# Kernel tuning notes

Measured on AMD Instinct MI355X. Metric: run time of the kernel, lower is better.

## Reference

```python
import jax, jax.numpy as jnp
import numpy as np

D_MODEL = 1024
NUM_HEADS = 16
HEAD_DIM = D_MODEL // NUM_HEADS


def setup_inputs() -> dict:
    key = jax.random.key(0)
    kx, kq, kk, kv, ko = jax.random.split(key, 5)
    init_std = float(np.sqrt(2.0 / (D_MODEL + D_MODEL)))
    def trunc(k):
        # trunc normal in [-3std, 3std], matching nn.init.trunc_normal_
        return jax.random.truncated_normal(k, -3.0, 3.0, (D_MODEL, D_MODEL), jnp.float32) * init_std
    return {
        "x": jax.random.normal(kx, (2, 2048, D_MODEL), jnp.float32),
        "Wq": trunc(kq),
        "Wk": trunc(kk),
        "Wv": trunc(kv),
        "Wo": trunc(ko),
    }


def reference(x, Wq, Wk, Wv, Wo):
    b, s, _ = x.shape
    # projections: Linear computes x @ W.T with W [out, in]
    q = (x @ Wq.T).reshape(b, s, NUM_HEADS, HEAD_DIM).transpose(0, 2, 1, 3)
    k = (x @ Wk.T).reshape(b, s, NUM_HEADS, HEAD_DIM).transpose(0, 2, 1, 3)
    v = (x @ Wv.T).reshape(b, s, NUM_HEADS, HEAD_DIM).transpose(0, 2, 1, 3)
    scale = 1.0 / jnp.sqrt(jnp.float32(HEAD_DIM))
    logits = jnp.einsum("bhqd,bhkd->bhqk", q, k)  # [b,h,s,s]
    causal = jnp.tril(jnp.ones((s, s), dtype=bool))
    logits = jnp.where(causal, logits, -jnp.inf)
    attn = jax.nn.softmax(logits * scale, axis=-1)
    out = jnp.einsum("bhqk,bhkd->bhqd", attn, v)
    out = out.transpose(0, 2, 1, 3).reshape(b, s, D_MODEL)
    return out @ Wo.T
```

## Files before the change

kernel.cpp:

```cpp
#include <hip/hip_runtime.h>
#include <hip/hip_bf16.h>


#define DEVI __device__ __forceinline__

typedef __bf16 bf16x8 __attribute__((ext_vector_type(8)));
typedef short  short8 __attribute__((ext_vector_type(8)));
typedef float  f32x4  __attribute__((ext_vector_type(4)));
typedef float  f32x16 __attribute__((ext_vector_type(16)));
typedef unsigned int u32x4 __attribute__((ext_vector_type(4)));

DEVI short f2bfs(float f) {
    __hip_bfloat16 h = __float2bfloat16(f);
    return __builtin_bit_cast(short, h);
}
DEVI unsigned pack2rb(float a, float b) {
    const unsigned ua = __builtin_bit_cast(unsigned, a) + 0x8000u;
    const unsigned ub = __builtin_bit_cast(unsigned, b) + 0x8000u;
    return __builtin_amdgcn_perm(ub, ua, 0x07060302u);
}
DEVI bf16x8 ld8(const short* p) {
    return __builtin_bit_cast(bf16x8, *(const short8*)p);
}
DEVI void gload16(const void* g, void* lds) {
    __builtin_amdgcn_global_load_lds(
        (const __attribute__((address_space(1))) void*)g,
        (__attribute__((address_space(3))) void*)lds, 16, 0, 0);
}
DEVI void plswap(unsigned& a, unsigned& b) {
    asm volatile("v_permlane32_swap_b32 %0, %1" : "+v"(a), "+v"(b));
}
DEVI const short* lds_swc(const short* base, int row, int col) {
    return (const short*)((const char*)base + (((row << 7) + (col << 1)) ^ ((row & 7) << 4)));
}

#if defined(__has_builtin)
#if __has_builtin(__builtin_amdgcn_exp2f)
#define HAVE_EXP2 1
#endif
#endif
DEVI float ex2(float x) {
#ifdef HAVE_EXP2
    return __builtin_amdgcn_exp2f(x);
#else
    return __expf(x * 0.69314718055994531f);
#endif
}
#define CEXP 0.18033688011112042f
#define MCF  (64.0f * CEXP)

__global__ __launch_bounds__(256) void convert_kernel(
    const float* __restrict__ x, const float* __restrict__ Wq,
    const float* __restrict__ Wk, const float* __restrict__ Wv,
    const float* __restrict__ Wo, short* __restrict__ xb, short* __restrict__ wb) {
    const int bid = blockIdx.x;
    const float* src;
    short* dst;
    int i8;
    if (bid < 2048) {
        src = x; dst = xb;
        i8 = (bid * 256 + threadIdx.x) * 8;
    } else {
        const int w = bid - 2048;
        const int z = w >> 9;
        src = (z == 0) ? Wq : (z == 1) ? Wk : (z == 2) ? Wv : Wo;
        dst = wb + (size_t)z * 1048576;
        i8 = (((w & 511) * 256) + threadIdx.x) * 8;
    }
    float4 a = ((const float4*)(src + i8))[0];
    float4 b = ((const float4*)(src + i8))[1];
    short8 t;
    t[0] = f2bfs(a.x); t[1] = f2bfs(a.y); t[2] = f2bfs(a.z); t[3] = f2bfs(a.w);
    t[4] = f2bfs(b.x); t[5] = f2bfs(b.y); t[6] = f2bfs(b.z); t[7] = f2bfs(b.w);
    *(short8*)(dst + i8) = t;
}

template <int BM, int BN, int MF, int NF, int WN>
DEVI void gemm_kloop64(const short* __restrict__ A, const short* __restrict__ B,
                       short* As, short* Bs, int wid, int lane, f32x4 acc[MF][NF]) {
    const int l15 = lane & 15, l4 = lane >> 4;
    const int wm = wid / WN, wn = wid % WN;
    const int rowc = lane >> 3;
    const int gcol = ((lane & 7) ^ rowc) * 8;
    constexpr int NCHA = BM / 8, NCHB = BN / 8;
#pragma unroll 1
    for (int k0 = 0; k0 < 1024; k0 += 64) {
        __syncthreads();
#pragma unroll
        for (int c = wid; c < NCHA; c += 4)
            gload16(A + (size_t)(c * 8 + rowc) * 1024 + k0 + gcol, As + c * 512);
#pragma unroll
        for (int c = wid; c < NCHB; c += 4)
            gload16(B + (size_t)(c * 8 + rowc) * 1024 + k0 + gcol, Bs + c * 512);
        __syncthreads();
#pragma unroll
        for (int kk = 0; kk < 2; ++kk) {
            bf16x8 af[MF], bf[NF];
#pragma unroll
            for (int m = 0; m < MF; ++m) {
                const int row = wm * (MF * 16) + m * 16 + l15;
                af[m] = ld8(As + row * 64 + (((kk * 4 + l4) ^ (row & 7)) * 8));
            }
#pragma unroll
            for (int n = 0; n < NF; ++n) {
                const int row = wn * (NF * 16) + n * 16 + l15;
                bf[n] = ld8(Bs + row * 64 + (((kk * 4 + l4) ^ (row & 7)) * 8));
            }
#pragma unroll
            for (int m = 0; m < MF; ++m)
#pragma unroll
                for (int n = 0; n < NF; ++n)
                    acc[m][n] = __builtin_amdgcn_mfma_f32_16x16x32_bf16(af[m], bf[n], acc[m][n], 0, 0, 0);
        }
    }
}

__global__ __launch_bounds__(256) void gemm_qkv_kernel(
    const short* __restrict__ xb, const short* __restrict__ wb,
    short* __restrict__ Qo, short* __restrict__ Ko, short* __restrict__ VtG) {
    __shared__ short As[8192], Bs[8192];
    const int tid = threadIdx.x, lane = tid & 63, wid = tid >> 6;
    const int l15 = lane & 15, l4 = lane >> 4;
    const int wm = wid >> 1, wn = wid & 1;
    const int y = blockIdx.y, wsel = y >> 3;
    const int row0 = blockIdx.x * 128, col0 = (y & 7) * 128;

    f32x4 acc[4][4] = {};
    gemm_kloop64<128, 128, 4, 4, 2>(
        xb + (size_t)row0 * 1024,
        wb + (size_t)wsel * 1048576 + (size_t)col0 * 1024,
        As, Bs, wid, lane, acc);

    if (wsel == 2) {
#pragma unroll
        for (int m = 0; m < 4; ++m)
#pragma unroll
            for (int n = 0; n < 4; ++n)
#pragma unroll
                for (int j = 0; j < 4; ++j) {
                    int row = row0 + wm * 64 + m * 16 + l4 * 4 + j;
                    int col = col0 + wn * 64 + n * 16 + l15;
                    VtG[(size_t)col * 4096 + row] = f2bfs(acc[m][n][j]);
                }
    } else {
        short* C = (wsel == 0) ? Qo : Ko;
#pragma unroll
        for (int m = 0; m < 4; ++m)
#pragma unroll
            for (int n = 0; n < 4; ++n)
#pragma unroll
                for (int j = 0; j < 4; ++j) {
                    int row = row0 + wm * 64 + m * 16 + l4 * 4 + j;
                    int col = col0 + wn * 64 + n * 16 + l15;
                    C[(size_t)row * 1024 + col] = f2bfs(acc[m][n][j]);
                }
    }
}

__global__ __launch_bounds__(256) void gemm_wo_kernel(
    const short* __restrict__ Ao, const short* __restrict__ Wob,
    float* __restrict__ Cout) {
    __shared__ short As[4096], Bs[8192];
    const int tid = threadIdx.x, lane = tid & 63, wid = tid >> 6;
    const int l15 = lane & 15, l4 = lane >> 4;
    const int wn = wid;
    const int row0 = blockIdx.x * 64, col0 = blockIdx.y * 128;

    f32x4 acc[4][2] = {};
    gemm_kloop64<64, 128, 4, 2, 4>(
        Ao + (size_t)row0 * 1024, Wob + (size_t)col0 * 1024,
        As, Bs, wid, lane, acc);

#pragma unroll
    for (int m = 0; m < 4; ++m)
#pragma unroll
        for (int n = 0; n < 2; ++n)
#pragma unroll
            for (int j = 0; j < 4; ++j) {
                int row = row0 + m * 16 + l4 * 4 + j;
                int col = col0 + wn * 32 + n * 16 + l15;
                Cout[(size_t)row * 1024 + col] = acc[m][n][j];
            }
}

DEVI void read_frags(const short* Ks, const short* Vts, int l31, int hi,
                     bf16x8 kf[8], bf16x8 vb[8]) {
#pragma unroll
    for (int ds = 0; ds < 4; ++ds) {
        kf[ds]     = ld8(lds_swc(Ks, l31,      ds * 16 + hi * 8));
        kf[4 + ds] = ld8(lds_swc(Ks, 32 + l31, ds * 16 + hi * 8));
    }
#pragma unroll
    for (int c = 0; c < 2; ++c) {
        vb[c * 4 + 0] = ld8(lds_swc(Vts, l31,      c * 32 + hi * 8));
        vb[c * 4 + 1] = ld8(lds_swc(Vts, 32 + l31, c * 32 + hi * 8));
        vb[c * 4 + 2] = ld8(lds_swc(Vts, l31,      c * 32 + 16 + hi * 8));
        vb[c * 4 + 3] = ld8(lds_swc(Vts, 32 + l31, c * 32 + 16 + hi * 8));
    }
}

template <bool DIAG>
DEVI void attn_tile_r(int kv0, const bf16x8 kf[8], const bf16x8 vb[8],
                      const bf16x8 qf[4], f32x16& o0, f32x16& o1,
                      float& l, int qrow, int hi) {
    f32x16 s0 = 0.0f, s1 = 0.0f;
    __builtin_amdgcn_s_setprio(1);
#pragma unroll
    for (int ds = 0; ds < 4; ++ds)
        s0 = __builtin_amdgcn_mfma_f32_32x32x16_bf16(kf[ds], qf[ds], s0, 0, 0, 0);
#pragma unroll
    for (int ds = 0; ds < 4; ++ds)
        s1 = __builtin_amdgcn_mfma_f32_32x32x16_bf16(kf[4 + ds], qf[ds], s1, 0, 0, 0);
    __builtin_amdgcn_s_setprio(0);

    if (DIAG) {
#pragma unroll
        for (int r = 0; r < 16; ++r) {
            const int kvr = kv0 + (r & 3) + 8 * (r >> 2) + 4 * hi;
            if (kvr > qrow)      s0[r] = -3.0e38f;
            if (kvr + 32 > qrow) s1[r] = -3.0e38f;
        }
    }

    float r0 = 0.f, r1 = 0.f, r2 = 0.f, r3 = 0.f;
    unsigned w0[8], w1[8];
#pragma unroll
    for (int i = 0; i < 8; ++i) {
        const float p0 = ex2(__builtin_fmaf(s0[2 * i],     CEXP, -MCF));
        const float p1 = ex2(__builtin_fmaf(s0[2 * i + 1], CEXP, -MCF));
        const float p2 = ex2(__builtin_fmaf(s1[2 * i],     CEXP, -MCF));
        const float p3 = ex2(__builtin_fmaf(s1[2 * i + 1], CEXP, -MCF));
        r0 += p0; r1 += p1; r2 += p2; r3 += p3;
        w0[i] = pack2rb(p0, p1);
        w1[i] = pack2rb(p2, p3);
    }
    l += (r0 + r1) + (r2 + r3);

    __builtin_amdgcn_s_setprio(1);
#pragma unroll
    for (int c = 0; c < 2; ++c) {
        const unsigned* w = (c == 0) ? w0 : w1;
        unsigned a0 = w[0], a2 = w[2]; plswap(a0, a2);
        unsigned a1 = w[1], a3 = w[3]; plswap(a1, a3);
        unsigned a4 = w[4], a6 = w[6]; plswap(a4, a6);
        unsigned a5 = w[5], a7 = w[7]; plswap(a5, a7);
        u32x4 lo, hw;
        lo[0] = a0; lo[1] = a1; lo[2] = a2; lo[3] = a3;
        hw[0] = a4; hw[1] = a5; hw[2] = a6; hw[3] = a7;
        const bf16x8 paL = __builtin_bit_cast(bf16x8, lo);
        const bf16x8 paH = __builtin_bit_cast(bf16x8, hw);

        o0 = __builtin_amdgcn_mfma_f32_32x32x16_bf16(paL, vb[c * 4 + 0], o0, 0, 0, 0);
        o1 = __builtin_amdgcn_mfma_f32_32x32x16_bf16(paL, vb[c * 4 + 1], o1, 0, 0, 0);
        o0 = __builtin_amdgcn_mfma_f32_32x32x16_bf16(paH, vb[c * 4 + 2], o0, 0, 0, 0);
        o1 = __builtin_amdgcn_mfma_f32_32x32x16_bf16(paH, vb[c * 4 + 3], o1, 0, 0, 0);
    }
    __builtin_amdgcn_s_setprio(0);
}

__global__ __launch_bounds__(128) void attn_kernel(
    const short* __restrict__ Q, const short* __restrict__ K,
    const short* __restrict__ VtG, short* __restrict__ O) {
    __shared__ short KsA[4096], VtsA[4096], KsB[4096], VtsB[4096];

    const int tid = threadIdx.x, lane = tid & 63, wid = tid >> 6;
    const int l31 = lane & 31, hi = lane >> 5;
    const int bid = blockIdx.x;
    const int qt = 31 - (bid >> 5);
    const int bh = bid & 31;
    const int b = bh >> 4, h = bh & 15;
    const size_t base = (size_t)b * 2048 * 1024 + (size_t)h * 64;
    const short* Qp = Q + base;
    const short* Kp = K + base;
    const short* Vp = VtG + (size_t)(h * 64) * 4096 + (size_t)b * 2048;
    short* Op = O + base;

    const int q0w = qt * 64 + wid * 32;
    const int qrow = q0w + l31;

    const int srw = lane >> 3;
    const int swc = ((lane & 7) ^ srw) * 8;
    const short* kSrc = Kp + (size_t)srw * 1024 + swc;
    const short* vSrc = Vp + (size_t)srw * 4096 + swc;
    const int cc0 = wid * 4;

#define ISSUE_TILE(Ksb, Vtsb, kv0_)                                           \
    {                                                                         \
        const int kv0i = (kv0_);                                              \
        _Pragma("unroll")                                                     \
        for (int c = 0; c < 4; ++c) {                                         \
            const int cc = cc0 + c;                                           \
            gload16(kSrc + (size_t)(kv0i + cc * 8) * 1024, (Ksb) + cc * 512); \
            gload16(vSrc + (size_t)(cc * 8) * 4096 + kv0i, (Vtsb) + cc * 512);\
        }                                                                     \
    }

    const int nt = qt + 1;

    ISSUE_TILE(KsA, VtsA, 0);

    bf16x8 qf[4];
#pragma unroll
    for (int ds = 0; ds < 4; ++ds)
        qf[ds] = ld8(Qp + (size_t)qrow * 1024 + ds * 16 + hi * 8);

    asm volatile("s_waitcnt vmcnt(0)" ::: "memory");
    __builtin_amdgcn_s_barrier();
    __builtin_amdgcn_sched_barrier(0);

    if (nt > 1) ISSUE_TILE(KsB, VtsB, 64);
    bf16x8 kf[8], vb[8];
    read_frags(KsA, VtsA, l31, hi, kf, vb);
    __builtin_amdgcn_sched_barrier(0);

    f32x16 o0 = 0.0f, o1 = 0.0f;
    float l = 0.0f;

#pragma unroll 1
    for (int t = 0; t < nt - 1; ++t) {
        attn_tile_r<false>(t * 64, kf, vb, qf, o0, o1, l, qrow, hi);
        asm volatile("s_waitcnt lgkmcnt(0) vmcnt(0)" ::: "memory");
        __builtin_amdgcn_s_barrier();
        __builtin_amdgcn_sched_barrier(0);
        if (t + 2 < nt) {
            short* Kso  = (t & 1) ? KsB  : KsA;
            short* Vtso = (t & 1) ? VtsB : VtsA;
            ISSUE_TILE(Kso, Vtso, (t + 2) * 64);
        }
        const short* Ksn  = (t & 1) ? KsA  : KsB;
        const short* Vtsn = (t & 1) ? VtsA : VtsB;
        read_frags(Ksn, Vtsn, l31, hi, kf, vb);
        __builtin_amdgcn_sched_barrier(0);
    }

    attn_tile_r<true>((nt - 1) * 64, kf, vb, qf, o0, o1, l, qrow, hi);
#undef ISSUE_TILE

    const float lt = l + __shfl_xor(l, 32, 64);
    const float il = 1.0f / lt;
#pragma unroll
    for (int r = 0; r < 16; ++r) {
        const int cr = (r & 3) + 8 * (r >> 2) + 4 * hi;
        const float s = __shfl(il, cr, 64);
        const size_t row = (size_t)(q0w + cr) * 1024;
        Op[row + l31]      = f2bfs(o0[r] * s);
        Op[row + 32 + l31] = f2bfs(o1[r] * s);
    }
}

extern "C" void kernel_launch(void* const* d_in, const int* in_sizes, int n_in,
                              void* d_out, int out_size, void* d_ws, size_t ws_size,
                              hipStream_t stream) {
    const float* x  = (const float*)d_in[0];
    const float* Wq = (const float*)d_in[1];
    const float* Wk = (const float*)d_in[2];
    const float* Wv = (const float*)d_in[3];
    const float* Wo = (const float*)d_in[4];

    short* wb  = (short*)d_ws;
    short* Qw  = wb + (size_t)4 * 1048576;
    short* Kw  = Qw + (size_t)4194304;
    short* Vtw = Kw + (size_t)4194304;
    short* xb  = (short*)d_out;

    convert_kernel<<<4096, 256, 0, stream>>>(x, Wq, Wk, Wv, Wo, xb, wb);
    gemm_qkv_kernel<<<dim3(32, 24), 256, 0, stream>>>(xb, wb, Qw, Kw, Vtw);
    attn_kernel<<<1024, 128, 0, stream>>>(Qw, Kw, Vtw, Qw);
    gemm_wo_kernel<<<dim3(64, 8), 256, 0, stream>>>(Qw, wb + (size_t)3 * 1048576, (float*)d_out);
}
```

Measured before the change: 116.1 us.

## Double-buffer GEMM k-loop and retile QKV projection with XCD-aware block mapping

The GEMM inner loop now double-buffers LDS tiles, issuing the next k-slice's global-to-LDS loads before computing on the current one, with a single barrier per iteration. The QKV kernel switches to 128x192 tiles over the fused 3072-wide weight matrix, launched as a 1D grid of 512 blocks. Blocks are remapped so that neighbouring column tiles land on the same XCD, and the epilogue routes each column to Q, K or transposed V. This costs more LDS (80KB dynamic) and more accumulator registers, which may reduce occupancy.

```diff
diff --git a/kernel.cpp b/kernel.cpp
--- a/kernel.cpp
+++ b/kernel.cpp
@@ -76,35 +76,51 @@
 }
 
 template <int BM, int BN, int MF, int NF, int WN>
-DEVI void gemm_kloop64(const short* __restrict__ A, const short* __restrict__ B,
-                       short* As, short* Bs, int wid, int lane, f32x4 acc[MF][NF]) {
+DEVI void gemm_kloop64_db(const short* __restrict__ A, const short* __restrict__ B,
+                          short* As0, short* Bs0, short* As1, short* Bs1,
+                          int wid, int lane, f32x4 acc[MF][NF]) {
     const int l15 = lane & 15, l4 = lane >> 4;
     const int wm = wid / WN, wn = wid % WN;
     const int rowc = lane >> 3;
     const int gcol = ((lane & 7) ^ rowc) * 8;
     constexpr int NCHA = BM / 8, NCHB = BN / 8;
+
+#define GISSUE(As_, Bs_, k0_)                                                  \
+    {                                                                          \
+        _Pragma("unroll")                                                      \
+        for (int c = wid; c < NCHA; c += 4)                                    \
+            gload16(A + (size_t)(c * 8 + rowc) * 1024 + (k0_) + gcol, (As_) + c * 512); \
+        _Pragma("unroll")                                                      \
+        for (int c = wid; c < NCHB; c += 4)                                    \
+            gload16(B + (size_t)(c * 8 + rowc) * 1024 + (k0_) + gcol, (Bs_) + c * 512); \
+    }
+
+    GISSUE(As0, Bs0, 0);
+    asm volatile("s_waitcnt vmcnt(0)" ::: "memory");
+    __builtin_amdgcn_s_barrier();
+    __builtin_amdgcn_sched_barrier(0);
+
 #pragma unroll 1
-    for (int k0 = 0; k0 < 1024; k0 += 64) {
-        __syncthreads();
-#pragma unroll
-        for (int c = wid; c < NCHA; c += 4)
-            gload16(A + (size_t)(c * 8 + rowc) * 1024 + k0 + gcol, As + c * 512);
-#pragma unroll
-        for (int c = wid; c < NCHB; c += 4)
-            gload16(B + (size_t)(c * 8 + rowc) * 1024 + k0 + gcol, Bs + c * 512);
-        __syncthreads();
+    for (int k = 0; k < 16; ++k) {
+        if (k + 1 < 16) {
+            short* Asn = (k & 1) ? As0 : As1;
+            short* Bsn = (k & 1) ? Bs0 : Bs1;
+            GISSUE(Asn, Bsn, (k + 1) * 64);
+        }
+        const short* Asc = (k & 1) ? As1 : As0;
+        const short* Bsc = (k & 1) ? Bs1 : Bs0;
 #pragma unroll
         for (int kk = 0; kk < 2; ++kk) {
             bf16x8 af[MF], bf[NF];
 #pragma unroll
             for (int m = 0; m < MF; ++m) {
                 const int row = wm * (MF * 16) + m * 16 + l15;
-                af[m] = ld8(As + row * 64 + (((kk * 4 + l4) ^ (row & 7)) * 8));
+                af[m] = ld8(Asc + row * 64 + (((kk * 4 + l4) ^ (row & 7)) * 8));
             }
 #pragma unroll
             for (int n = 0; n < NF; ++n) {
                 const int row = wn * (NF * 16) + n * 16 + l15;
-                bf[n] = ld8(Bs + row * 64 + (((kk * 4 + l4) ^ (row & 7)) * 8));
+                bf[n] = ld8(Bsc + row * 64 + (((kk * 4 + l4) ^ (row & 7)) * 8));
             }
 #pragma unroll
             for (int m = 0; m < MF; ++m)
@@ -112,64 +128,64 @@
                 for (int n = 0; n < NF; ++n)
                     acc[m][n] = __builtin_amdgcn_mfma_f32_16x16x32_bf16(af[m], bf[n], acc[m][n], 0, 0, 0);
         }
-    }
+        asm volatile("s_waitcnt lgkmcnt(0) vmcnt(0)" ::: "memory");
+        __builtin_amdgcn_s_barrier();
+        __builtin_amdgcn_sched_barrier(0);
+    }
+#undef GISSUE
 }
 
 __global__ __launch_bounds__(256) void gemm_qkv_kernel(
     const short* __restrict__ xb, const short* __restrict__ wb,
     short* __restrict__ Qo, short* __restrict__ Ko, short* __restrict__ VtG) {
-    __shared__ short As[8192], Bs[8192];
+    extern __shared__ short smem[];
+    short* As0 = smem;
+    short* As1 = smem + 8192;
+    short* Bs0 = smem + 16384;
+    short* Bs1 = smem + 28672;
+
     const int tid = threadIdx.x, lane = tid & 63, wid = tid >> 6;
     const int l15 = lane & 15, l4 = lane >> 4;
     const int wm = wid >> 1, wn = wid & 1;
-    const int y = blockIdx.y, wsel = y >> 3;
-    const int row0 = blockIdx.x * 128, col0 = (y & 7) * 128;
-
-    f32x4 acc[4][4] = {};
-    gemm_kloop64<128, 128, 4, 4, 2>(
-        xb + (size_t)row0 * 1024,
-        wb + (size_t)wsel * 1048576 + (size_t)col0 * 1024,
-        As, Bs, wid, lane, acc);
-
-    if (wsel == 2) {
-#pragma unroll
-        for (int m = 0; m < 4; ++m)
-#pragma unroll
-            for (int n = 0; n < 4; ++n)
-#pragma unroll
-                for (int j = 0; j < 4; ++j) {
-                    int row = row0 + wm * 64 + m * 16 + l4 * 4 + j;
-                    int col = col0 + wn * 64 + n * 16 + l15;
-                    VtG[(size_t)col * 4096 + row] = f2bfs(acc[m][n][j]);
-                }
-    } else {
-        short* C = (wsel == 0) ? Qo : Ko;
-#pragma unroll
-        for (int m = 0; m < 4; ++m)
-#pragma unroll
-            for (int n = 0; n < 4; ++n)
-#pragma unroll
-                for (int j = 0; j < 4; ++j) {
-                    int row = row0 + wm * 64 + m * 16 + l4 * 4 + j;
-                    int col = col0 + wn * 64 + n * 16 + l15;
-                    C[(size_t)row * 1024 + col] = f2bfs(acc[m][n][j]);
-                }
-    }
+    const int bid = blockIdx.x;
+    const int xcd = bid & 7, idx = bid >> 3;
+    const int ytile = xcd * 2 + (idx & 1);
+    const int xtile = idx >> 1;
+    const int row0 = xtile * 128, col0 = ytile * 192;
+
+    f32x4 acc[4][6] = {};
+    gemm_kloop64_db<128, 192, 4, 6, 2>(
+        xb + (size_t)row0 * 1024, wb + (size_t)col0 * 1024,
+        As0, Bs0, As1, Bs1, wid, lane, acc);
+
+#pragma unroll
+    for (int m = 0; m < 4; ++m)
+#pragma unroll
+        for (int n = 0; n < 6; ++n)
+#pragma unroll
+            for (int j = 0; j < 4; ++j) {
+                const int row = row0 + wm * 64 + m * 16 + l4 * 4 + j;
+                const int col = col0 + wn * 96 + n * 16 + l15;
+                const short v = f2bfs(acc[m][n][j]);
+                if (col < 1024)       Qo[(size_t)row * 1024 + col] = v;
+                else if (col < 2048)  Ko[(size_t)row * 1024 + (col - 1024)] = v;
+                else                  VtG[(size_t)(col - 2048) * 4096 + row] = v;
+            }
 }
 
 __global__ __launch_bounds__(256) void gemm_wo_kernel(
     const short* __restrict__ Ao, const short* __restrict__ Wob,
     float* __restrict__ Cout) {
-    __shared__ short As[4096], Bs[8192];
+    __shared__ short As0[4096], As1[4096], Bs0[8192], Bs1[8192];
     const int tid = threadIdx.x, lane = tid & 63, wid = tid >> 6;
     const int l15 = lane & 15, l4 = lane >> 4;
     const int wn = wid;
     const int row0 = blockIdx.x * 64, col0 = blockIdx.y * 128;
 
     f32x4 acc[4][2] = {};
-    gemm_kloop64<64, 128, 4, 2, 4>(
+    gemm_kloop64_db<64, 128, 4, 2, 4>(
         Ao + (size_t)row0 * 1024, Wob + (size_t)col0 * 1024,
-        As, Bs, wid, lane, acc);
+        As0, Bs0, As1, Bs1, wid, lane, acc);
 
 #pragma unroll
     for (int m = 0; m < 4; ++m)
@@ -177,8 +193,8 @@
         for (int n = 0; n < 2; ++n)
 #pragma unroll
             for (int j = 0; j < 4; ++j) {
-                int row = row0 + m * 16 + l4 * 4 + j;
-                int col = col0 + wn * 32 + n * 16 + l15;
+                const int row = row0 + m * 16 + l4 * 4 + j;
+                const int col = col0 + wn * 32 + n * 16 + l15;
                 Cout[(size_t)row * 1024 + col] = acc[m][n][j];
             }
 }
@@ -364,7 +380,7 @@
     short* xb  = (short*)d_out;
 
     convert_kernel<<<4096, 256, 0, stream>>>(x, Wq, Wk, Wv, Wo, xb, wb);
-    gemm_qkv_kernel<<<dim3(32, 24), 256, 0, stream>>>(xb, wb, Qw, Kw, Vtw);
+    gemm_qkv_kernel<<<512, 256, 81920, stream>>>(xb, wb, Qw, Kw, Vtw);
     attn_kernel<<<1024, 128, 0, stream>>>(Qw, Kw, Vtw, Qw);
     gemm_wo_kernel<<<dim3(64, 8), 256, 0, stream>>>(Qw, wb + (size_t)3 * 1048576, (float*)d_out);
 }
```

Measured after the change: 127.2 us. 1.1x slower.

## Process two KV tiles per barrier with four-stage LDS ring

Applied to the files above, without the earlier changes.

The attention kernel now keeps four K/V tile buffers in LDS and handles two 64-key tiles per loop iteration, loading fragments for both before computing. This halves the number of waitcnt+barrier synchronisations per KV tile and prefetches two tiles ahead. In exchange LDS use doubles to 64KB per block and register pressure rises from holding two sets of K/V fragments, which may reduce occupancy or cause spills.

```diff
diff --git a/kernel.cpp b/kernel.cpp
--- a/kernel.cpp
+++ b/kernel.cpp
@@ -177,8 +177,8 @@
         for (int n = 0; n < 2; ++n)
 #pragma unroll
             for (int j = 0; j < 4; ++j) {
-                int row = row0 + m * 16 + l4 * 4 + j;
-                int col = col0 + wn * 32 + n * 16 + l15;
+                const int row = row0 + m * 16 + l4 * 4 + j;
+                const int col = col0 + wn * 32 + n * 16 + l15;
                 Cout[(size_t)row * 1024 + col] = acc[m][n][j];
             }
 }
@@ -261,7 +261,7 @@
 __global__ __launch_bounds__(128) void attn_kernel(
     const short* __restrict__ Q, const short* __restrict__ K,
     const short* __restrict__ VtG, short* __restrict__ O) {
-    __shared__ short KsA[4096], VtsA[4096], KsB[4096], VtsB[4096];
+    __shared__ short Kb[4][4096], Vb[4][4096];
 
     const int tid = threadIdx.x, lane = tid & 63, wid = tid >> 6;
     const int l31 = lane & 31, hi = lane >> 5;
@@ -284,20 +284,22 @@
     const short* vSrc = Vp + (size_t)srw * 4096 + swc;
     const int cc0 = wid * 4;
 
-#define ISSUE_TILE(Ksb, Vtsb, kv0_)                                           \
-    {                                                                         \
-        const int kv0i = (kv0_);                                              \
-        _Pragma("unroll")                                                     \
-        for (int c = 0; c < 4; ++c) {                                         \
-            const int cc = cc0 + c;                                           \
-            gload16(kSrc + (size_t)(kv0i + cc * 8) * 1024, (Ksb) + cc * 512); \
-            gload16(vSrc + (size_t)(cc * 8) * 4096 + kv0i, (Vtsb) + cc * 512);\
-        }                                                                     \
-    }
-
     const int nt = qt + 1;
 
-    ISSUE_TILE(KsA, VtsA, 0);
+#define ISS(i)                                                                 \
+    if ((i) < nt) {                                                            \
+        short* Ksb = Kb[(i) & 3];                                              \
+        short* Vsb = Vb[(i) & 3];                                              \
+        const int kv0i = (i) * 64;                                             \
+        _Pragma("unroll")                                                      \
+        for (int c = 0; c < 4; ++c) {                                          \
+            const int cc = cc0 + c;                                            \
+            gload16(kSrc + (size_t)(kv0i + cc * 8) * 1024, Ksb + cc * 512);    \
+            gload16(vSrc + (size_t)(cc * 8) * 4096 + kv0i, Vsb + cc * 512);    \
+        }                                                                      \
+    }
+
+    ISS(0); ISS(1);
 
     bf16x8 qf[4];
 #pragma unroll
@@ -308,33 +310,37 @@
     __builtin_amdgcn_s_barrier();
     __builtin_amdgcn_sched_barrier(0);
 
-    if (nt > 1) ISSUE_TILE(KsB, VtsB, 64);
-    bf16x8 kf[8], vb[8];
-    read_frags(KsA, VtsA, l31, hi, kf, vb);
+    bf16x8 kf0[8], vb0[8], kf1[8], vb1[8];
+    read_frags(Kb[0], Vb[0], l31, hi, kf0, vb0);
+    if (nt > 1) read_frags(Kb[1], Vb[1], l31, hi, kf1, vb1);
     __builtin_amdgcn_sched_barrier(0);
+    ISS(2); ISS(3);
 
     f32x16 o0 = 0.0f, o1 = 0.0f;
     float l = 0.0f;
 
+    int t = 0;
 #pragma unroll 1
-    for (int t = 0; t < nt - 1; ++t) {
-        attn_tile_r<false>(t * 64, kf, vb, qf, o0, o1, l, qrow, hi);
-        asm volatile("s_waitcnt lgkmcnt(0) vmcnt(0)" ::: "memory");
-        __builtin_amdgcn_s_barrier();
-        __builtin_amdgcn_sched_barrier(0);
-        if (t + 2 < nt) {
-            short* Kso  = (t & 1) ? KsB  : KsA;
-            short* Vtso = (t & 1) ? VtsB : VtsA;
-            ISSUE_TILE(Kso, Vtso, (t + 2) * 64);
+    while (t + 1 < nt) {
+        attn_tile_r<false>(t * 64, kf0, vb0, qf, o0, o1, l, qrow, hi);
+        if (t + 1 == nt - 1)
+            attn_tile_r<true>((t + 1) * 64, kf1, vb1, qf, o0, o1, l, qrow, hi);
+        else
+            attn_tile_r<false>((t + 1) * 64, kf1, vb1, qf, o0, o1, l, qrow, hi);
+        t += 2;
+        if (t < nt) {
+            asm volatile("s_waitcnt lgkmcnt(0) vmcnt(0)" ::: "memory");
+            __builtin_amdgcn_s_barrier();
+            __builtin_amdgcn_sched_barrier(0);
+            read_frags(Kb[t & 3], Vb[t & 3], l31, hi, kf0, vb0);
+            if (t + 1 < nt) read_frags(Kb[(t + 1) & 3], Vb[(t + 1) & 3], l31, hi, kf1, vb1);
+            __builtin_amdgcn_sched_barrier(0);
+            ISS(t + 2); ISS(t + 3);
         }
-        const short* Ksn  = (t & 1) ? KsA  : KsB;
-        const short* Vtsn = (t & 1) ? VtsA : VtsB;
-        read_frags(Ksn, Vtsn, l31, hi, kf, vb);
-        __builtin_amdgcn_sched_barrier(0);
-    }
-
-    attn_tile_r<true>((nt - 1) * 64, kf, vb, qf, o0, o1, l, qrow, hi);
-#undef ISSUE_TILE
+    }
+    if (t < nt)
+        attn_tile_r<true>(t * 64, kf0, vb0, qf, o0, o1, l, qrow, hi);
+#undef ISS
 
     const float lt = l + __shfl_xor(l, 32, 64);
     const float il = 1.0f / lt;
```

Result: faster. 107.7 us (-7.2%).
